# Performance work log

Measured on AMD Instinct MI355X. Metric: run time of the kernel, lower is better.

Reference implementation:

```python
import jax, jax.numpy as jnp
import numpy as np

EPS = 1e-8


def setup_inputs() -> dict:
    key = jax.random.key(0)
    k1, k2, k3, k4 = jax.random.split(key, 4)
    B, Cin, Cout, K, S, H, W = 8, 512, 512, 3, 512, 64, 64
    return {
        "x": jax.random.normal(k1, (B, Cin, H, W), dtype=jnp.float32),
        "style": jax.random.normal(k2, (B, S), dtype=jnp.float32),
        "weight": jax.random.normal(k3, (1, Cout, Cin, K, K), dtype=jnp.float32),
        "mod_w": jax.random.normal(k4, (Cin, S), dtype=jnp.float32),
        "mod_b": jnp.ones((Cin,), dtype=jnp.float32),
    }


def reference(x, style, weight, mod_w, mod_b):
    B, Cin, H, W = x.shape
    Cout, K = weight.shape[1], weight.shape[-1]
    style_dim = mod_w.shape[1]
    conv_scale = 1.0 / np.sqrt(Cin * K * K)  # 1/sqrt(fan_in)
    mod_scale = 1.0 / np.sqrt(style_dim)     # EqualLinear scale (lr_mul=1)

    # EqualLinear modulation: (B, Cin)
    s = style @ (mod_w * mod_scale).T + mod_b

    # per-sample modulated weights: (B, Cout, Cin, K, K)
    w = conv_scale * weight * s[:, None, :, None, None]
    demod = jax.lax.rsqrt(jnp.sum(w * w, axis=(2, 3, 4)) + EPS)  # (B, Cout)
    w = w * demod[:, :, None, None, None]

    # grouped conv with groups = batch
    w = w.reshape(B * Cout, Cin, K, K)
    xg = x.reshape(1, B * Cin, H, W)
    pad = (K - 1) // 2
    out = jax.lax.conv_general_dilated(
        xg, w,
        window_strides=(1, 1),
        padding=[(pad, pad), (pad, pad)],
        dimension_numbers=("NCHW", "OIHW", "NCHW"),
        feature_group_count=B,
    )
    return out.reshape(B, Cout, out.shape[2], out.shape[3])
```

## Files before the change

kernel.cpp:

```cpp
#include <hip/hip_runtime.h>
#include <hip/hip_bf16.h>
#include <cstdint>
#include <cstddef>

typedef __bf16 bf16x8 __attribute__((ext_vector_type(8)));
typedef float f32x4 __attribute__((ext_vector_type(4)));
typedef unsigned int uintx4 __attribute__((ext_vector_type(4)));

#define CONV_SCALE 0.014731391274719738f
#define MOD_SCALE  0.044194173824159216f

__device__ __forceinline__ unsigned short f2bf(float v) {
  unsigned int u = __float_as_uint(v);
  return (unsigned short)((u + 0x7FFFu + ((u >> 16) & 1u)) >> 16);
}

__device__ __forceinline__ void gload16(const void* g, void* l) {
  __builtin_amdgcn_global_load_lds(
      (const __attribute__((address_space(1))) unsigned int*)g,
      (__attribute__((address_space(3))) unsigned int*)l, 16, 0, 0);
}

__global__ void k_modulate(const float* __restrict__ style,
                           const float* __restrict__ mod_w,
                           const float* __restrict__ mod_b,
                           float* __restrict__ s) {
  int blk = blockIdx.x;
  int b = blk >> 2, ch = blk & 3;
  int t = threadIdx.x;
  int ci = ch * 128 + (t >> 1), half = t & 1;
  const float* st = style + b * 512 + half * 256;
  const float* mw = mod_w + (size_t)ci * 512 + half * 256;
  float acc = 0.f;
  #pragma unroll 8
  for (int k = 0; k < 256; k += 4) {
    f32x4 a = *(const f32x4*)(st + k);
    f32x4 m = *(const f32x4*)(mw + k);
    acc += a[0] * m[0] + a[1] * m[1] + a[2] * m[2] + a[3] * m[3];
  }
  acc += __shfl_xor(acc, 1);
  if (half == 0) s[b * 512 + ci] = acc * MOD_SCALE + mod_b[ci];
}

__global__ void k_wTq(const float* __restrict__ weight,
                      unsigned short* __restrict__ wT,
                      float* __restrict__ wsq) {
  __shared__ float lds[4608];
  int co = blockIdx.x;
  int t = threadIdx.x;
  const float* w = weight + (size_t)co * 4608;
  #pragma unroll
  for (int i = 0; i < 18; ++i) lds[t + i * 256] = w[t + i * 256];
  __syncthreads();
  for (int i = t; i < 576; i += 256) {
    int tap = i / 64, c8 = (i & 63) * 8;
    union { uintx4 v; unsigned short us[8]; } pk;
    #pragma unroll
    for (int j = 0; j < 8; ++j) pk.us[j] = f2bf(lds[(c8 + j) * 9 + tap]);
    *(uintx4*)(wT + ((size_t)tap * 512 + co) * 512 + c8) = pk.v;
  }
  for (int ci = t; ci < 512; ci += 256) {
    float a = 0.f;
    #pragma unroll
    for (int tap = 0; tap < 9; ++tap) { float v = lds[ci * 9 + tap]; a += v * v; }
    wsq[co * 512 + ci] = a * (CONV_SCALE * CONV_SCALE);
  }
}

__global__ void k_demod(const float* __restrict__ wsq, const float* __restrict__ s,
                        float* __restrict__ demod) {
  int b = blockIdx.x;
  int co = threadIdx.x;
  const float* wq = wsq + (size_t)co * 512;
  const float* sb = s + b * 512;
  float acc = 0.f;
  #pragma unroll 4
  for (int ci = 0; ci < 512; ci += 4) {
    f32x4 q = *(const f32x4*)(wq + ci);
    f32x4 v = *(const f32x4*)(sb + ci);
    acc += q[0] * v[0] * v[0] + q[1] * v[1] * v[1] + q[2] * v[2] * v[2] + q[3] * v[3] * v[3];
  }
  demod[b * 512 + co] = rsqrtf(acc + 1e-8f);
}

__global__ void k_xT(const float* __restrict__ x, const float* __restrict__ s,
                     unsigned short* __restrict__ xT) {
  __shared__ float lds[128][68];
  int cc = blockIdx.x;
  int h = blockIdx.y;
  int b = blockIdx.z;
  int t = threadIdx.x;
  int w4 = (t & 15) * 4, rr = t >> 4;
  #pragma unroll
  for (int i = 0; i < 8; ++i) {
    int ci = i * 16 + rr;
    *(f32x4*)&lds[ci][w4] =
        *(const f32x4*)&x[(((size_t)(b * 512 + cc * 128 + ci)) * 64 + h) * 64 + w4];
  }
  __syncthreads();
  int pos = t >> 2, c4 = t & 3;
  #pragma unroll
  for (int q = 0; q < 4; ++q) {
    int cb = q * 32 + c4 * 8;
    union { uintx4 v; unsigned short us[8]; } pk;
    #pragma unroll
    for (int j = 0; j < 8; ++j) {
      int ci = cb + j;
      pk.us[j] = f2bf(lds[ci][pos] * s[b * 512 + cc * 128 + ci]);
    }
    *(uintx4*)(xT + (((size_t)(b * 64 + h)) * 64 + pos) * 512 + cc * 128 + cb) = pk.v;
  }
}

__global__ __launch_bounds__(512, 2) void k_conv(
    const unsigned short* __restrict__ xT,
    const unsigned short* __restrict__ wT,
    const float* __restrict__ demod,
    float* __restrict__ out) {
  extern __shared__ __align__(16) char lds_raw[];
  char* xb0   = lds_raw;
  char* xb1   = lds_raw + 42240;
  char* wring = lds_raw + 84480;
  char* trash = lds_raw + 117248;

  const int id  = blockIdx.x;
  const int g_ord = (id & 7) * 32 + (id >> 3);
  const int co_t  = g_ord >> 6;
  const int slice = g_ord & 63;
  const int b   = slice >> 3;
  const int h_t = slice & 7;

  const int t = threadIdx.x;
  const int lane = t & 63, wv = t >> 6;
  const int h0  = h_t * 8;
  const int co0 = co_t * 128;
  const int l15 = lane & 15, kg = lane >> 4;
  const int wrow = wv & 3;
  const int wco  = wv >> 2;

  {
    uintx4 z = {0u, 0u, 0u, 0u};
    for (int i = t; i < 5280; i += 512) ((uintx4*)lds_raw)[i] = z;
  }
  __syncthreads();

  auto xstage = [&](int j, int ccs, char* xbuf) {
    int r = j >> 2, k = j & 3;
    int hh = h0 - 1 + r;
    int hc = ((unsigned)hh < 64u) ? hh : 0;
    int p = r * 66 + 1 + k * 16 + (lane >> 2);
    const void* src = xT + (((size_t)(b * 64 + hc)) * 64 + k * 16 + (lane >> 2)) * 512
                      + ccs * 32 + (((lane & 3) ^ ((p >> 1) & 3)) << 3);
    void* dst = ((unsigned)hh < 64u) ? (void*)(xbuf + (r * 66 + 1 + k * 16) * 64)
                                     : (void*)trash;
    gload16(src, dst);
  };
  auto wstage = [&](int g) {
    int gc = (g <= 143) ? g : 143;
    int s = g & 3;
    int cc2 = gc / 9, tap2 = gc - cc2 * 9;
    int row0 = wv * 16;
    int row = row0 + (lane >> 2);
    const void* src = wT + ((size_t)tap2 * 512 + co0 + row) * 512
                      + cc2 * 32 + (((lane & 3) ^ ((row >> 1) & 3)) << 3);
    void* dst = (g <= 143) ? (void*)(wring + s * 8192 + row0 * 64) : (void*)trash;
    gload16(src, dst);
  };

  f32x4 acc[4][2][4] = {};

  #pragma unroll
  for (int i = 0; i < 5; ++i) xstage(wv * 5 + i, 0, xb0);
  wstage(0);
  wstage(1);
  __syncthreads();

  #pragma unroll 1
  for (int cc = 0; cc < 16; ++cc) {
    const char* xcur = (cc & 1) ? xb1 : xb0;
    char* xnxt = (cc & 1) ? xb0 : xb1;
    const int ccs = (cc + 1) & 15;
    #pragma unroll
    for (int tap = 0; tap < 9; ++tap) {
      if (tap == 0 || tap == 1 || tap == 7 || tap == 8)
        asm volatile("s_waitcnt vmcnt(1)" ::: "memory");
      else
        asm volatile("s_waitcnt vmcnt(2)" ::: "memory");

      const int g = cc * 9 + tap;
      const int s = g & 3;
      const int dh = tap / 3, dw = tap % 3;

      bf16x8 af[4], bfr[2][4];
      #pragma unroll
      for (int m = 0; m < 4; ++m) {
        int row = wco * 64 + m * 16 + l15;
        af[m] = *(const bf16x8*)(wring + s * 8192 + row * 64 + ((kg ^ ((row >> 1) & 3)) << 4));
      }
      #pragma unroll
      for (int r = 0; r < 2; ++r)
        #pragma unroll
        for (int n = 0; n < 4; ++n) {
          int p = (2 * wrow + r + dh) * 66 + n * 16 + l15 + dw;
          bfr[r][n] = *(const bf16x8*)(xcur + p * 64 + ((kg ^ ((p >> 1) & 3)) << 4));
        }

      wstage(g + 2);
      if (tap >= 1 && tap <= 5) xstage((tap - 1) * 8 + wv, ccs, xnxt);

      __builtin_amdgcn_s_barrier();

      __builtin_amdgcn_s_setprio(1);
      #pragma unroll
      for (int m = 0; m < 4; ++m)
        #pragma unroll
        for (int r = 0; r < 2; ++r)
          #pragma unroll
          for (int n = 0; n < 4; ++n)
            acc[m][r][n] = __builtin_amdgcn_mfma_f32_16x16x32_bf16(af[m], bfr[r][n], acc[m][r][n], 0, 0, 0);
      __builtin_amdgcn_s_setprio(0);
    }
  }

  #pragma unroll
  for (int m = 0; m < 4; ++m) {
    #pragma unroll
    for (int q = 0; q < 4; ++q) {
      int co = co0 + wco * 64 + m * 16 + kg * 4 + q;
      float scl = CONV_SCALE * demod[b * 512 + co];
      #pragma unroll
      for (int r = 0; r < 2; ++r) {
        int h_out = h0 + 2 * wrow + r;
        #pragma unroll
        for (int n = 0; n < 4; ++n) {
          out[(((size_t)(b * 512 + co)) * 64 + h_out) * 64 + n * 16 + l15] = acc[m][r][n][q] * scl;
        }
      }
    }
  }
}

extern "C" void kernel_launch(void* const* d_in, const int* in_sizes, int n_in,
                              void* d_out, int out_size, void* d_ws, size_t ws_size,
                              hipStream_t stream) {
  const float* x      = (const float*)d_in[0];
  const float* style  = (const float*)d_in[1];
  const float* weight = (const float*)d_in[2];
  const float* mod_w  = (const float*)d_in[3];
  const float* mod_b  = (const float*)d_in[4];
  float* out = (float*)d_out;

  char* ws = (char*)d_ws;
  unsigned short* xT = (unsigned short*)ws;
  unsigned short* wT = (unsigned short*)(ws + 33554432);
  float* s     = (float*)(ws + 38273024);
  float* wsq   = (float*)(ws + 38289408);
  float* demod = (float*)(ws + 39337984);

  static int lds_set = 0;
  if (!lds_set) {
    (void)hipFuncSetAttribute((const void*)k_conv,
                              hipFuncAttributeMaxDynamicSharedMemorySize, 118272);
    lds_set = 1;
  }

  hipLaunchKernelGGL(k_modulate, dim3(32),       dim3(256), 0, stream, style, mod_w, mod_b, s);
  hipLaunchKernelGGL(k_wTq,      dim3(512),      dim3(256), 0, stream, weight, wT, wsq);
  hipLaunchKernelGGL(k_demod,    dim3(8),        dim3(512), 0, stream, wsq, s, demod);
  hipLaunchKernelGGL(k_xT,       dim3(4, 64, 8), dim3(256), 0, stream, x, s, xT);
  hipLaunchKernelGGL(k_conv,     dim3(256),      dim3(512), 118272, stream, xT, wT, demod, out);
}
```

Before: 183.2 us.

## Batch conv taps into three-tap phases with six-slot weight ring and fuse prep kernels

The conv main loop now processes three taps per phase with a single barrier and wait, instead of one barrier per tap. Weight staging moves to a six-slot LDS ring so three future taps can be prefetched while the current three are consumed. Separately, the four prep kernels are merged into two launches by dispatching on block index. This is meant to cut barrier and wait stalls and launch overhead, at the cost of more LDS per block and more live fragment registers.

Result: slower. 319.3 us (+74.4%).

```diff
diff --git a/kernel.cpp b/kernel.cpp
--- a/kernel.cpp
+++ b/kernel.cpp
@@ -21,96 +21,119 @@
       (__attribute__((address_space(3))) unsigned int*)l, 16, 0, 0);
 }
 
-__global__ void k_modulate(const float* __restrict__ style,
-                           const float* __restrict__ mod_w,
-                           const float* __restrict__ mod_b,
-                           float* __restrict__ s) {
-  int blk = blockIdx.x;
-  int b = blk >> 2, ch = blk & 3;
+__global__ void k_prep1(const float* __restrict__ style,
+                        const float* __restrict__ mod_w,
+                        const float* __restrict__ mod_b,
+                        const float* __restrict__ weight,
+                        float* __restrict__ s,
+                        unsigned short* __restrict__ wT,
+                        float* __restrict__ wsq) {
+  __shared__ float lds[4608];
   int t = threadIdx.x;
-  int ci = ch * 128 + (t >> 1), half = t & 1;
-  const float* st = style + b * 512 + half * 256;
-  const float* mw = mod_w + (size_t)ci * 512 + half * 256;
-  float acc = 0.f;
-  #pragma unroll 8
-  for (int k = 0; k < 256; k += 4) {
-    f32x4 a = *(const f32x4*)(st + k);
-    f32x4 m = *(const f32x4*)(mw + k);
-    acc += a[0] * m[0] + a[1] * m[1] + a[2] * m[2] + a[3] * m[3];
-  }
-  acc += __shfl_xor(acc, 1);
-  if (half == 0) s[b * 512 + ci] = acc * MOD_SCALE + mod_b[ci];
-}
-
-__global__ void k_wTq(const float* __restrict__ weight,
-                      unsigned short* __restrict__ wT,
-                      float* __restrict__ wsq) {
-  __shared__ float lds[4608];
-  int co = blockIdx.x;
+  if (blockIdx.x < 512) {
+    int co = blockIdx.x;
+    const float* w = weight + (size_t)co * 4608;
+    #pragma unroll
+    for (int i = 0; i < 18; ++i) lds[t + i * 256] = w[t + i * 256];
+    __syncthreads();
+    for (int i = t; i < 576; i += 256) {
+      int tap = i / 64, c8 = (i & 63) * 8;
+      union { uintx4 v; unsigned short us[8]; } pk;
+      #pragma unroll
+      for (int j = 0; j < 8; ++j) pk.us[j] = f2bf(lds[(c8 + j) * 9 + tap]);
+      *(uintx4*)(wT + ((size_t)tap * 512 + co) * 512 + c8) = pk.v;
+    }
+    for (int ci = t; ci < 512; ci += 256) {
+      float a = 0.f;
+      #pragma unroll
+      for (int tap = 0; tap < 9; ++tap) { float v = lds[ci * 9 + tap]; a += v * v; }
+      wsq[co * 512 + ci] = a * (CONV_SCALE * CONV_SCALE);
+    }
+  } else {
+    int blk = blockIdx.x - 512;
+    int b = blk >> 2, ch = blk & 3;
+    int ci = ch * 128 + (t >> 1), half = t & 1;
+    const float* st = style + b * 512 + half * 256;
+    const float* mw = mod_w + (size_t)ci * 512 + half * 256;
+    float acc = 0.f;
+    #pragma unroll 8
+    for (int k = 0; k < 256; k += 4) {
+      f32x4 a = *(const f32x4*)(st + k);
+      f32x4 m = *(const f32x4*)(mw + k);
+      acc += a[0] * m[0] + a[1] * m[1] + a[2] * m[2] + a[3] * m[3];
+    }
+    acc += __shfl_xor(acc, 1);
+    if (half == 0) s[b * 512 + ci] = acc * MOD_SCALE + mod_b[ci];
+  }
+}
+
+__global__ void k_prep2(const float* __restrict__ x,
+                        const float* __restrict__ s,
+                        const float* __restrict__ wsq,
+                        unsigned short* __restrict__ xT,
+                        float* __restrict__ demod) {
+  __shared__ float lds[128][68];
   int t = threadIdx.x;
-  const float* w = weight + (size_t)co * 4608;
-  #pragma unroll
-  for (int i = 0; i < 18; ++i) lds[t + i * 256] = w[t + i * 256];
-  __syncthreads();
-  for (int i = t; i < 576; i += 256) {
-    int tap = i / 64, c8 = (i & 63) * 8;
-    union { uintx4 v; unsigned short us[8]; } pk;
-    #pragma unroll
-    for (int j = 0; j < 8; ++j) pk.us[j] = f2bf(lds[(c8 + j) * 9 + tap]);
-    *(uintx4*)(wT + ((size_t)tap * 512 + co) * 512 + c8) = pk.v;
-  }
-  for (int ci = t; ci < 512; ci += 256) {
-    float a = 0.f;
-    #pragma unroll
-    for (int tap = 0; tap < 9; ++tap) { float v = lds[ci * 9 + tap]; a += v * v; }
-    wsq[co * 512 + ci] = a * (CONV_SCALE * CONV_SCALE);
-  }
-}
-
-__global__ void k_demod(const float* __restrict__ wsq, const float* __restrict__ s,
-                        float* __restrict__ demod) {
-  int b = blockIdx.x;
-  int co = threadIdx.x;
-  const float* wq = wsq + (size_t)co * 512;
-  const float* sb = s + b * 512;
-  float acc = 0.f;
-  #pragma unroll 4
-  for (int ci = 0; ci < 512; ci += 4) {
-    f32x4 q = *(const f32x4*)(wq + ci);
-    f32x4 v = *(const f32x4*)(sb + ci);
-    acc += q[0] * v[0] * v[0] + q[1] * v[1] * v[1] + q[2] * v[2] * v[2] + q[3] * v[3] * v[3];
-  }
-  demod[b * 512 + co] = rsqrtf(acc + 1e-8f);
-}
-
-__global__ void k_xT(const float* __restrict__ x, const float* __restrict__ s,
-                     unsigned short* __restrict__ xT) {
-  __shared__ float lds[128][68];
-  int cc = blockIdx.x;
-  int h = blockIdx.y;
-  int b = blockIdx.z;
-  int t = threadIdx.x;
-  int w4 = (t & 15) * 4, rr = t >> 4;
-  #pragma unroll
-  for (int i = 0; i < 8; ++i) {
-    int ci = i * 16 + rr;
-    *(f32x4*)&lds[ci][w4] =
-        *(const f32x4*)&x[(((size_t)(b * 512 + cc * 128 + ci)) * 64 + h) * 64 + w4];
-  }
-  __syncthreads();
-  int pos = t >> 2, c4 = t & 3;
-  #pragma unroll
-  for (int q = 0; q < 4; ++q) {
-    int cb = q * 32 + c4 * 8;
-    union { uintx4 v; unsigned short us[8]; } pk;
-    #pragma unroll
-    for (int j = 0; j < 8; ++j) {
-      int ci = cb + j;
-      pk.us[j] = f2bf(lds[ci][pos] * s[b * 512 + cc * 128 + ci]);
-    }
-    *(uintx4*)(xT + (((size_t)(b * 64 + h)) * 64 + pos) * 512 + cc * 128 + cb) = pk.v;
-  }
-}
+  int id = blockIdx.x;
+  if (id < 2048) {
+    int cc = id & 3, h = (id >> 2) & 63, b = id >> 8;
+    int w4 = (t & 15) * 4, rr = t >> 4;
+    #pragma unroll
+    for (int i = 0; i < 8; ++i) {
+      int ci = i * 16 + rr;
+      *(f32x4*)&lds[ci][w4] =
+          *(const f32x4*)&x[(((size_t)(b * 512 + cc * 128 + ci)) * 64 + h) * 64 + w4];
+    }
+    __syncthreads();
+    int pos = t >> 2, c4 = t & 3;
+    #pragma unroll
+    for (int q = 0; q < 4; ++q) {
+      int cb = q * 32 + c4 * 8;
+      union { uintx4 v; unsigned short us[8]; } pk;
+      #pragma unroll
+      for (int j = 0; j < 8; ++j) {
+        int ci = cb + j;
+        pk.us[j] = f2bf(lds[ci][pos] * s[b * 512 + cc * 128 + ci]);
+      }
+      *(uintx4*)(xT + (((size_t)(b * 64 + h)) * 64 + pos) * 512 + cc * 128 + cb) = pk.v;
+    }
+  } else {
+    int blk = id - 2048;
+    int b = blk >> 1;
+    int co = (blk & 1) * 256 + t;
+    const float* wq = wsq + (size_t)co * 512;
+    const float* sb = s + b * 512;
+    float acc = 0.f;
+    #pragma unroll 4
+    for (int ci = 0; ci < 512; ci += 4) {
+      f32x4 q = *(const f32x4*)(wq + ci);
+      f32x4 v = *(const f32x4*)(sb + ci);
+      acc += q[0] * v[0] * v[0] + q[1] * v[1] * v[1] + q[2] * v[2] * v[2] + q[3] * v[3] * v[3];
+    }
+    demod[b * 512 + co] = rsqrtf(acc + 1e-8f);
+  }
+}
+
+#define READ_FRAGS(G, DH, DW, AF, BF) do {                                        \
+  const char* wb_ = wring + ((G) % 6) * 8192;                                     \
+  _Pragma("unroll") for (int m_ = 0; m_ < 4; ++m_) {                              \
+    int row_ = wco * 64 + m_ * 16 + l15;                                          \
+    AF[m_] = *(const bf16x8*)(wb_ + row_ * 64 + ((kg ^ ((row_ >> 1) & 3)) << 4)); } \
+  _Pragma("unroll") for (int r_ = 0; r_ < 2; ++r_)                                \
+    _Pragma("unroll") for (int n_ = 0; n_ < 4; ++n_) {                            \
+      int p_ = (2 * wrow + r_ + (DH)) * 66 + n_ * 16 + l15 + (DW);                \
+      BF[r_][n_] = *(const bf16x8*)(xcur + p_ * 64 + ((kg ^ ((p_ >> 1) & 3)) << 4)); } \
+} while (0)
+
+#define DO_MFMA(AF, BF) do {                                                      \
+  __builtin_amdgcn_s_setprio(1);                                                  \
+  _Pragma("unroll") for (int m_ = 0; m_ < 4; ++m_)                                \
+    _Pragma("unroll") for (int r_ = 0; r_ < 2; ++r_)                              \
+      _Pragma("unroll") for (int n_ = 0; n_ < 4; ++n_)                            \
+        acc[m_][r_][n_] = __builtin_amdgcn_mfma_f32_16x16x32_bf16(                \
+            AF[m_], BF[r_][n_], acc[m_][r_][n_], 0, 0, 0);                        \
+  __builtin_amdgcn_s_setprio(0);                                                  \
+} while (0)
 
 __global__ __launch_bounds__(512, 2) void k_conv(
     const unsigned short* __restrict__ xT,
@@ -121,7 +144,7 @@
   char* xb0   = lds_raw;
   char* xb1   = lds_raw + 42240;
   char* wring = lds_raw + 84480;
-  char* trash = lds_raw + 117248;
+  char* trash = lds_raw + 133632;
 
   const int id  = blockIdx.x;
   const int g_ord = (id & 7) * 32 + (id >> 3);
@@ -157,23 +180,21 @@
   };
   auto wstage = [&](int g) {
     int gc = (g <= 143) ? g : 143;
-    int s = g & 3;
+    int sl = gc % 6;
     int cc2 = gc / 9, tap2 = gc - cc2 * 9;
     int row0 = wv * 16;
     int row = row0 + (lane >> 2);
     const void* src = wT + ((size_t)tap2 * 512 + co0 + row) * 512
                       + cc2 * 32 + (((lane & 3) ^ ((row >> 1) & 3)) << 3);
-    void* dst = (g <= 143) ? (void*)(wring + s * 8192 + row0 * 64) : (void*)trash;
+    void* dst = (g <= 143) ? (void*)(wring + sl * 8192 + row0 * 64) : (void*)trash;
     gload16(src, dst);
   };
 
   f32x4 acc[4][2][4] = {};
 
+  wstage(0); wstage(1); wstage(2);
   #pragma unroll
-  for (int i = 0; i < 5; ++i) xstage(wv * 5 + i, 0, xb0);
-  wstage(0);
-  wstage(1);
-  __syncthreads();
+  for (int i = 0; i < 5; ++i) xstage(wv + 8 * i, 0, xb0);
 
   #pragma unroll 1
   for (int cc = 0; cc < 16; ++cc) {
@@ -181,44 +202,25 @@
     char* xnxt = (cc & 1) ? xb0 : xb1;
     const int ccs = (cc + 1) & 15;
     #pragma unroll
-    for (int tap = 0; tap < 9; ++tap) {
-      if (tap == 0 || tap == 1 || tap == 7 || tap == 8)
-        asm volatile("s_waitcnt vmcnt(1)" ::: "memory");
-      else
-        asm volatile("s_waitcnt vmcnt(2)" ::: "memory");
-
-      const int g = cc * 9 + tap;
-      const int s = g & 3;
-      const int dh = tap / 3, dw = tap % 3;
-
-      bf16x8 af[4], bfr[2][4];
-      #pragma unroll
-      for (int m = 0; m < 4; ++m) {
-        int row = wco * 64 + m * 16 + l15;
-        af[m] = *(const bf16x8*)(wring + s * 8192 + row * 64 + ((kg ^ ((row >> 1) & 3)) << 4));
-      }
-      #pragma unroll
-      for (int r = 0; r < 2; ++r)
-        #pragma unroll
-        for (int n = 0; n < 4; ++n) {
-          int p = (2 * wrow + r + dh) * 66 + n * 16 + l15 + dw;
-          bfr[r][n] = *(const bf16x8*)(xcur + p * 64 + ((kg ^ ((p >> 1) & 3)) << 4));
-        }
-
-      wstage(g + 2);
-      if (tap >= 1 && tap <= 5) xstage((tap - 1) * 8 + wv, ccs, xnxt);
-
+    for (int ph = 0; ph < 3; ++ph) {
+      if (ph == 0) asm volatile("s_waitcnt vmcnt(0)" ::: "memory");
+      else         asm volatile("s_waitcnt vmcnt(2)" ::: "memory");
       __builtin_amdgcn_s_barrier();
 
-      __builtin_amdgcn_s_setprio(1);
-      #pragma unroll
-      for (int m = 0; m < 4; ++m)
-        #pragma unroll
-        for (int r = 0; r < 2; ++r)
-          #pragma unroll
-          for (int n = 0; n < 4; ++n)
-            acc[m][r][n] = __builtin_amdgcn_mfma_f32_16x16x32_bf16(af[m], bfr[r][n], acc[m][r][n], 0, 0, 0);
-      __builtin_amdgcn_s_setprio(0);
+      const int g0 = cc * 9 + ph * 3;
+      bf16x8 af0[4], bf0[2][4];
+      READ_FRAGS(g0, ph, 0, af0, bf0);
+      wstage(g0 + 3); wstage(g0 + 4); wstage(g0 + 5);
+      if (ph == 0)      { xstage(wv,      ccs, xnxt); xstage(wv + 8,  ccs, xnxt); }
+      else if (ph == 1) { xstage(wv + 16, ccs, xnxt); xstage(wv + 24, ccs, xnxt); }
+      else              { xstage(wv + 32, ccs, xnxt); }
+      DO_MFMA(af0, bf0);
+      bf16x8 af1[4], bf1[2][4];
+      READ_FRAGS(g0 + 1, ph, 1, af1, bf1);
+      DO_MFMA(af1, bf1);
+      bf16x8 af2[4], bf2[2][4];
+      READ_FRAGS(g0 + 2, ph, 2, af2, bf2);
+      DO_MFMA(af2, bf2);
     }
   }
 
@@ -260,13 +262,12 @@
   static int lds_set = 0;
   if (!lds_set) {
     (void)hipFuncSetAttribute((const void*)k_conv,
-                              hipFuncAttributeMaxDynamicSharedMemorySize, 118272);
+                              hipFuncAttributeMaxDynamicSharedMemorySize, 134656);
     lds_set = 1;
   }
 
-  hipLaunchKernelGGL(k_modulate, dim3(32),       dim3(256), 0, stream, style, mod_w, mod_b, s);
-  hipLaunchKernelGGL(k_wTq,      dim3(512),      dim3(256), 0, stream, weight, wT, wsq);
-  hipLaunchKernelGGL(k_demod,    dim3(8),        dim3(512), 0, stream, wsq, s, demod);
-  hipLaunchKernelGGL(k_xT,       dim3(4, 64, 8), dim3(256), 0, stream, x, s, xT);
-  hipLaunchKernelGGL(k_conv,     dim3(256),      dim3(512), 118272, stream, xT, wT, demod, out);
-}
+  hipLaunchKernelGGL(k_prep1, dim3(544),  dim3(256), 0, stream,
+                     style, mod_w, mod_b, weight, s, wT, wsq);
+  hipLaunchKernelGGL(k_prep2, dim3(2064), dim3(256), 0, stream, x, s, wsq, xT, demod);
+  hipLaunchKernelGGL(k_conv,  dim3(256),  dim3(512), 134656, stream, xT, wT, demod, out);
+}
```
